# Performance work log

Measured on AMD Instinct MI355X. Metric: run time of the kernel, lower is better.

## Reference

```python
import jax, jax.numpy as jnp
import numpy as np

B, IC2, N, K = 8, 128, 2048, 32   # x: [B, 2*in_channels, N, k]
C, G = 64, 8                       # out_channels, groups
CPG = C // G                       # channels per group
EPS_BN = 1e-5


def conv1x1(x, w, b=None):
    # 1x1 conv over [B, Cin, N, K] with weight [Cout, Cin]
    y = jnp.einsum('oc,bcnk->bonk', w, x)
    if b is not None:
        y = y + b[None, :, None, None]
    return y


def bn(x, g, beta, m, v):
    # inference-mode BatchNorm2d
    scale = g / jnp.sqrt(v + EPS_BN)
    return x * scale[None, :, None, None] + (beta - m * scale)[None, :, None, None]


def lrelu(x):
    return jax.nn.leaky_relu(x, 0.2)


def setup_inputs() -> dict:
    key = jax.random.key(0)
    ks = jax.random.split(key, 32)
    d = {}
    d['x'] = jax.random.normal(ks[0], (B, IC2, N, K), jnp.float32)
    d['rel_pos'] = jax.random.normal(ks[1], (B, 3, N, K), jnp.float32)
    # pos_net
    d['pos_w1'] = jax.random.normal(ks[2], (C, 3), jnp.float32) * 0.1
    d['pos_bn_g'] = jax.random.uniform(ks[3], (C,), jnp.float32, 0.5, 1.5)
    d['pos_bn_b'] = jax.random.normal(ks[4], (C,), jnp.float32) * 0.1
    d['pos_bn_m'] = jax.random.normal(ks[5], (C,), jnp.float32) * 0.1
    d['pos_bn_v'] = jax.random.uniform(ks[6], (C,), jnp.float32, 0.5, 1.5)
    d['pos_w2'] = jax.random.normal(ks[7], (C, C), jnp.float32) * 0.1
    d['pos_b2'] = jax.random.normal(ks[8], (C,), jnp.float32) * 0.1
    # pe_proj
    d['pe_w'] = jax.random.normal(ks[9], (G, C), jnp.float32) * 0.1
    d['pe_b'] = jax.random.normal(ks[10], (G,), jnp.float32) * 0.1
    # trans (Conv+BN+LeakyReLU)
    d['trans_w'] = jax.random.normal(ks[11], (C, IC2), jnp.float32) * 0.1
    d['trans_bn_g'] = jax.random.uniform(ks[12], (C,), jnp.float32, 0.5, 1.5)
    d['trans_bn_b'] = jax.random.normal(ks[13], (C,), jnp.float32) * 0.1
    d['trans_bn_m'] = jax.random.normal(ks[14], (C,), jnp.float32) * 0.1
    d['trans_bn_v'] = jax.random.uniform(ks[15], (C,), jnp.float32, 0.5, 1.5)
    # gate_net (hidden 16)
    d['gate_w1'] = jax.random.normal(ks[16], (16, IC2), jnp.float32) * 0.1
    d['gate_bn_g'] = jax.random.uniform(ks[17], (16,), jnp.float32, 0.5, 1.5)
    d['gate_bn_b'] = jax.random.normal(ks[18], (16,), jnp.float32) * 0.1
    d['gate_bn_m'] = jax.random.normal(ks[19], (16,), jnp.float32) * 0.1
    d['gate_bn_v'] = jax.random.uniform(ks[20], (16,), jnp.float32, 0.5, 1.5)
    d['gate_w2'] = jax.random.normal(ks[21], (1, 16), jnp.float32) * 0.1
    d['gate_b2'] = jnp.full((1,), 2.0, jnp.float32)  # init.constant_(bias, 2.0)
    # attn_net (hidden C//4 = 16)
    d['attn_w1'] = jax.random.normal(ks[22], (C // 4, IC2), jnp.float32) * 0.1
    d['attn_bn_g'] = jax.random.uniform(ks[23], (C // 4,), jnp.float32, 0.5, 1.5)
    d['attn_bn_b'] = jax.random.normal(ks[24], (C // 4,), jnp.float32) * 0.1
    d['attn_bn_m'] = jax.random.normal(ks[25], (C // 4,), jnp.float32) * 0.1
    d['attn_bn_v'] = jax.random.uniform(ks[26], (C // 4,), jnp.float32, 0.5, 1.5)
    d['attn_w2'] = jax.random.normal(ks[27], (G, C // 4), jnp.float32) * 0.1
    d['attn_b2'] = jax.random.normal(ks[28], (G,), jnp.float32) * 0.1
    return d


def reference(x, rel_pos, pos_w1, pos_bn_g, pos_bn_b, pos_bn_m, pos_bn_v, pos_w2, pos_b2,
              pe_w, pe_b, trans_w, trans_bn_g, trans_bn_b, trans_bn_m, trans_bn_v,
              gate_w1, gate_bn_g, gate_bn_b, gate_bn_m, gate_bn_v, gate_w2, gate_b2,
              attn_w1, attn_bn_g, attn_bn_b, attn_bn_m, attn_bn_v, attn_w2, attn_b2):
    # pos_net: conv -> BN -> LeakyReLU -> conv(bias)
    pos_enc = conv1x1(lrelu(bn(conv1x1(rel_pos, pos_w1), pos_bn_g, pos_bn_b, pos_bn_m, pos_bn_v)),
                      pos_w2, pos_b2)                                    # [B,C,N,K]
    # trans: conv -> BN -> LeakyReLU, plus positional encoding
    trans_feat = lrelu(bn(conv1x1(x, trans_w), trans_bn_g, trans_bn_b, trans_bn_m, trans_bn_v)) + pos_enc
    # gate_net (dropout=identity in eval): -> sigmoid gate [B,1,N,K]
    gate_h = lrelu(bn(conv1x1(x, gate_w1), gate_bn_g, gate_bn_b, gate_bn_m, gate_bn_v))
    gate_map = jax.nn.sigmoid(conv1x1(gate_h, gate_w2, gate_b2))
    # attn_net -> grouped logits [B,G,N,K]
    attn_h = lrelu(bn(conv1x1(x, attn_w1), attn_bn_g, attn_bn_b, attn_bn_m, attn_bn_v))
    attn_logits = conv1x1(attn_h, attn_w2, attn_b2)
    attn_logits = attn_logits + conv1x1(pos_enc, pe_w, pe_b)             # pe_proj
    attn_logits = attn_logits + jnp.log(gate_map + 1e-6)                 # full mode: log-combine gate
    attn_w = jax.nn.softmax(attn_logits, axis=-1)                        # softmax over neighbors k
    attn_w_exp = jnp.repeat(attn_w, CPG, axis=1)                         # repeat_interleave -> [B,C,N,K]
    out_attn = jnp.sum(trans_feat * attn_w_exp, axis=-1)                 # [B,C,N]
    out_max = jnp.max(trans_feat * gate_map, axis=-1)                    # [B,C,N]
    return out_attn + out_max
```

## Files before the change

### kernel.cpp

```cpp
#include <hip/hip_runtime.h>


typedef __attribute__((ext_vector_type(8))) short bf16x8;
typedef __attribute__((ext_vector_type(4))) float f32x4;

#define EPS_BN 1e-5f

__device__ __forceinline__ unsigned pk2(float a, float b){
  unsigned ua = __float_as_uint(a) + 0x8000u;
  unsigned ub = __float_as_uint(b) + 0x8000u;
  return __builtin_amdgcn_perm(ub, ua, 0x07060302);
}
__device__ __forceinline__ short f2bf(float a){
  unsigned u = __float_as_uint(a);
  u += 0x7FFFu + ((u >> 16) & 1u);
  return (short)(u >> 16);
}
__device__ __forceinline__ float lrelu(float v){ return fmaxf(v, 0.2f*v); }

__device__ __forceinline__ void st8(short* dst, float4 a, float4 b){
  *(uint2*)(dst)     = make_uint2(pk2(a.x,a.y), pk2(a.z,a.w));
  *(uint2*)(dst + 4) = make_uint2(pk2(b.x,b.y), pk2(b.z,b.w));
}
__device__ __forceinline__ bf16x8 ld8(const short* p){
  union { bf16x8 v; uint2 q[2]; } w;
  w.q[0] = *(const uint2*)(p);
  w.q[1] = *(const uint2*)(p + 4);
  return w.v;
}

template<int N>
__device__ __forceinline__ float ror16(float x){
  return __int_as_float(__builtin_amdgcn_mov_dpp(__float_as_int(x), 0x120+N, 0xF, 0xF, false));
}
__device__ __forceinline__ float rsum16(float v){
  v += ror16<1>(v); v += ror16<2>(v); v += ror16<4>(v); v += ror16<8>(v); return v;
}
__device__ __forceinline__ float rmax16(float v){
  v = fmaxf(v, ror16<1>(v)); v = fmaxf(v, ror16<2>(v));
  v = fmaxf(v, ror16<4>(v)); v = fmaxf(v, ror16<8>(v)); return v;
}

#define MFMA16(a,b,c) __builtin_amdgcn_mfma_f32_16x16x32_bf16((a),(b),(c),0,0,0)

__global__ void gsl_prep(const float* __restrict__ pos_w2, const float* __restrict__ pe_w,
                         const float* __restrict__ pe_b,   const float* __restrict__ pos_b2,
                         float* __restrict__ ws){
  int t = threadIdx.x;
  int r = t >> 6, j = t & 63;
  float s = 0.f;
  for (int c = 0; c < 64; ++c) s += pe_w[r*64 + c] * pos_w2[c*64 + j];
  ws[t] = s;
  if (t < 16){
    float v = 0.f;
    if (t < 8){
      v = pe_b[t];
      for (int c = 0; c < 64; ++c) v += pe_w[t*64 + c] * pos_b2[c];
    }
    ws[512 + t] = v;
  }
}

__global__ __launch_bounds__(256, 2)
void gsl_fused(const float* __restrict__ x,       const float* __restrict__ rel_pos,
               const float* __restrict__ pos_w1,  const float* __restrict__ pos_g,
               const float* __restrict__ pos_bb,  const float* __restrict__ pos_m,
               const float* __restrict__ pos_v,   const float* __restrict__ pos_w2,
               const float* __restrict__ pos_b2,  const float* __restrict__ trans_w,
               const float* __restrict__ tr_g,    const float* __restrict__ tr_bb,
               const float* __restrict__ tr_m,    const float* __restrict__ tr_v,
               const float* __restrict__ gate_w1, const float* __restrict__ ga_g,
               const float* __restrict__ ga_bb,   const float* __restrict__ ga_m,
               const float* __restrict__ ga_v,    const float* __restrict__ gate_w2,
               const float* __restrict__ gate_b2, const float* __restrict__ attn_w1,
               const float* __restrict__ at_g,    const float* __restrict__ at_bb,
               const float* __restrict__ at_m,    const float* __restrict__ at_v,
               const float* __restrict__ attn_w2, const float* __restrict__ attn_b2,
               const float* __restrict__ ws,      float* __restrict__ out)
{
  __shared__ __align__(16) char smem[70784];
  short* xbuf  = (short*)smem;
  short* wmain = (short*)(smem + 33792);
  short* wpos2 = (short*)(smem + 59136);
  float* trQ  = (float*)(smem + 68928);
  float* p1T  = (float*)(smem + 69952);
  float* gaT  = (float*)(smem + 70464);
  float* atT  = (float*)(smem + 70592);

  const int tid = threadIdx.x;
  const int wv  = tid >> 6;
  const int l   = tid & 63;
  const int l15 = l & 15, g4 = l >> 4;
  const int bid = blockIdx.x;
  const int b    = bid >> 6;
  const int nblk = (bid & 63) << 5;

  if (tid < 192){
    int r = tid >> 1, c0 = (tid & 1) * 64;
    const float* src = (r < 64) ? (trans_w + r*128)
                     : (r < 80) ? (gate_w1 + (r-64)*128)
                                : (attn_w1 + (r-80)*128);
    src += c0;
    short* dst = wmain + r*132 + c0;
    #pragma unroll
    for (int j = 0; j < 8; ++j)
      st8(dst + 8*j, *(const float4*)(src + 8*j), *(const float4*)(src + 8*j + 4));
  } else {
    int r = tid - 192;
    const float* src = pos_w2 + r*64;
    short* dst = wpos2 + r*68;
    #pragma unroll
    for (int j = 0; j < 8; ++j)
      st8(dst + 8*j, *(const float4*)(src + 8*j), *(const float4*)(src + 8*j + 4));
  }
  if (tid < 16){
    int r = tid >> 1, c0 = (tid & 1) * 32;
    const float* src = ws + r*64 + c0;
    short* dst = wpos2 + (64 + r)*68 + c0;
    #pragma unroll
    for (int j = 0; j < 4; ++j)
      st8(dst + 8*j, *(const float4*)(src + 8*j), *(const float4*)(src + 8*j + 4));
  }
  if (tid < 64){
    float s = tr_g[tid] * rsqrtf(tr_v[tid] + EPS_BN);
    *(float4*)(trQ + 4*tid) = make_float4(s, tr_bb[tid] - tr_m[tid]*s, pos_b2[tid], 0.f);
    float s2 = pos_g[tid] * rsqrtf(pos_v[tid] + EPS_BN);
    p1T[2*tid] = s2; p1T[2*tid+1] = pos_bb[tid] - pos_m[tid]*s2;
  } else if (tid < 80){
    int c = tid - 64;
    float s = ga_g[c] * rsqrtf(ga_v[c] + EPS_BN);
    gaT[2*c] = s; gaT[2*c+1] = ga_bb[c] - ga_m[c]*s;
  } else if (tid < 96){
    int c = tid - 80;
    float s = at_g[c] * rsqrtf(at_v[c] + EPS_BN);
    atT[2*c] = s; atT[2*c+1] = at_bb[c] - at_m[c]*s;
  }

  uint2 pw1p[4];
  #pragma unroll
  for (int m2 = 0; m2 < 4; ++m2){
    uint2 t = make_uint2(0u, 0u);
    if (g4 == 0){
      const float* rp = pos_w1 + (16*m2 + l15)*3;
      t.x = pk2(rp[0], rp[1]);
      t.y = pk2(rp[2], 0.f);
    }
    pw1p[m2] = t;
  }
  bf16x8 gaf;
  {
    bf16x8 t = {0,0,0,0,0,0,0,0};
    #pragma unroll
    for (int j = 0; j < 8; ++j){
      int k = 8*g4 + j;
      float v2 = 0.f;
      if (l15 < 8)       { if (k >= 16) v2 = attn_w2[l15*16 + (k-16)]; }
      else if (l15 == 8) { if (k < 16)  v2 = gate_w2[k]; }
      t[j] = f2bf(v2);
    }
    gaf = t;
  }
  const float gb2v = gate_b2[0];
  float lcr[4];
  #pragma unroll
  for (int r = 0; r < 4; ++r){
    int row = 4*g4 + r;
    lcr[r] = ws[512 + row] + ((row < 8) ? attn_b2[row] : 0.f);
  }

  const int col0 = 32*wv + l15, col1 = col0 + 16;
  const int lc0 = l15, lc1 = l15 + 16;
  const int lq = l & 7, ld = l >> 3;
  const int colb = 32*wv + 4*lq;
  char*  slice = smem + wv*8448;
  short* h1b   = (short*)slice;
  short* gab   = (short*)(slice + 4352);
  const float* xp0 = x + (((long)(b*128 + 8*ld)) << 16) + colb;
  const float* rpb = rel_pos + (((long)(3*b)) << 16);
  const int och = 16*(l15 >> 2) + 4*g4 + (l15 & 3);
  float* outb = out + (((long)(b*64 + och)) << 11) + nblk + wv;

  f32x4 fa[8], fb[8];
  float rc[6] = {0.f,0.f,0.f,0.f,0.f,0.f};
  {
    const long sb0 = (long)nblk * 32;
    #pragma unroll
    for (int j = 0; j < 8; ++j) fa[j] = *(const f32x4*)(xp0 + sb0 + (((long)j) << 16));
    #pragma unroll
    for (int j = 0; j < 8; ++j) fb[j] = *(const f32x4*)(xp0 + sb0 + (((long)(64+j)) << 16));
    if (g4 == 0){
      long sg = sb0 + col0;
      rc[0] = rpb[sg];          rc[1] = rpb[sg + 65536];      rc[2] = rpb[sg + 131072];
      rc[3] = rpb[sg + 16];     rc[4] = rpb[sg + 65536 + 16]; rc[5] = rpb[sg + 131072 + 16];
    }
  }

  __syncthreads();

  for (int it = 0; it < 8; ++it){
    const long sbase = (long)nblk*32 + 128*it;

    #pragma unroll
    for (int i2 = 0; i2 < 4; ++i2){
      short* dst = xbuf + (colb+i2)*132 + 8*ld;
      *(uint2*)(dst)      = make_uint2(pk2(fa[0][i2],fa[1][i2]), pk2(fa[2][i2],fa[3][i2]));
      *(uint2*)(dst + 4)  = make_uint2(pk2(fa[4][i2],fa[5][i2]), pk2(fa[6][i2],fa[7][i2]));
      *(uint2*)(dst + 64) = make_uint2(pk2(fb[0][i2],fb[1][i2]), pk2(fb[2][i2],fb[3][i2]));
      *(uint2*)(dst + 68) = make_uint2(pk2(fb[4][i2],fb[5][i2]), pk2(fb[6][i2],fb[7][i2]));
    }

    const long nsb = sbase + 128;
    if (it < 7){
      #pragma unroll
      for (int j = 0; j < 8; ++j) fa[j] = *(const f32x4*)(xp0 + nsb + (((long)j) << 16));
    }

    f32x4 acc[6][2];
    #pragma unroll
    for (int m = 0; m < 6; ++m){
      f32x4 z = {0.f,0.f,0.f,0.f};
      acc[m][0] = z; acc[m][1] = z;
    }
    #pragma unroll
    for (int ks = 0; ks < 4; ++ks){
      bf16x8 b0 = ld8(xbuf + col0*132 + 32*ks + 8*g4);
      bf16x8 b1 = ld8(xbuf + col1*132 + 32*ks + 8*g4);
      #pragma unroll
      for (int m = 0; m < 6; ++m){
        bf16x8 af = ld8(wmain + (16*m + l15)*132 + 32*ks + 8*g4);
        acc[m][0] = MFMA16(af, b0, acc[m][0]);
        acc[m][1] = MFMA16(af, b1, acc[m][1]);
      }
    }

    if (it < 7){
      #pragma unroll
      for (int j = 0; j < 8; ++j) fb[j] = *(const f32x4*)(xp0 + nsb + (((long)(64+j)) << 16));
    }

    {
      bf16x8 rf0 = {0,0,0,0,0,0,0,0}, rf1 = {0,0,0,0,0,0,0,0};
      if (g4 == 0){
        union { bf16x8 v; unsigned u[4]; } t0, t1;
        t0.u[0] = pk2(rc[0], rc[1]); t0.u[1] = pk2(rc[2], 0.f); t0.u[2] = 0u; t0.u[3] = 0u;
        t1.u[0] = pk2(rc[3], rc[4]); t1.u[1] = pk2(rc[5], 0.f); t1.u[2] = 0u; t1.u[3] = 0u;
        rf0 = t0.v; rf1 = t1.v;
      }
      #pragma unroll
      for (int m2 = 0; m2 < 4; ++m2){
        union { bf16x8 v; unsigned u[4]; } aw;
        aw.u[0] = pw1p[m2].x; aw.u[1] = pw1p[m2].y; aw.u[2] = 0u; aw.u[3] = 0u;
        f32x4 z = {0.f,0.f,0.f,0.f};
        f32x4 d0 = MFMA16(aw.v, rf0, z);
        f32x4 d1 = MFMA16(aw.v, rf1, z);
        int cb2 = 16*m2 + 4*g4;
        float2 t0 = *(const float2*)(p1T + 2*(cb2+0));
        float2 t1 = *(const float2*)(p1T + 2*(cb2+1));
        float2 t2 = *(const float2*)(p1T + 2*(cb2+2));
        float2 t3 = *(const float2*)(p1T + 2*(cb2+3));
        float h0 = lrelu(t0.x*d0[0]+t0.y), h1v = lrelu(t1.x*d0[1]+t1.y);
        float h2 = lrelu(t2.x*d0[2]+t2.y), h3 = lrelu(t3.x*d0[3]+t3.y);
        *(uint2*)(h1b + lc0*68 + cb2) = make_uint2(pk2(h0,h1v), pk2(h2,h3));
        h0 = lrelu(t0.x*d1[0]+t0.y); h1v = lrelu(t1.x*d1[1]+t1.y);
        h2 = lrelu(t2.x*d1[2]+t2.y); h3 = lrelu(t3.x*d1[3]+t3.y);
        *(uint2*)(h1b + lc1*68 + cb2) = make_uint2(pk2(h0,h1v), pk2(h2,h3));
      }
    }
    if (g4 == 0 && it < 7){
      long sg = nsb + col0;
      rc[0] = rpb[sg];          rc[1] = rpb[sg + 65536];      rc[2] = rpb[sg + 131072];
      rc[3] = rpb[sg + 16];     rc[4] = rpb[sg + 65536 + 16]; rc[5] = rpb[sg + 131072 + 16];
    }

    #pragma unroll
    for (int m = 0; m < 4; ++m)
      #pragma unroll
      for (int r = 0; r < 4; ++r){
        float4 tq = *(const float4*)(trQ + 4*(16*m + 4*g4 + r));
        acc[m][0][r] = lrelu(tq.x*acc[m][0][r] + tq.y) + tq.z;
        acc[m][1][r] = lrelu(tq.x*acc[m][1][r] + tq.y) + tq.z;
      }

    f32x4 pac4[2];
    {
      f32x4 z = {0.f,0.f,0.f,0.f};
      pac4[0] = z; pac4[1] = z;
    }
    #pragma unroll
    for (int ks = 0; ks < 2; ++ks){
      bf16x8 h0 = ld8(h1b + lc0*68 + 32*ks + 8*g4);
      bf16x8 h1v = ld8(h1b + lc1*68 + 32*ks + 8*g4);
      #pragma unroll
      for (int m2 = 0; m2 < 4; ++m2){
        bf16x8 af = ld8(wpos2 + (16*m2 + l15)*68 + 32*ks + 8*g4);
        acc[m2][0] = MFMA16(af, h0, acc[m2][0]);
        acc[m2][1] = MFMA16(af, h1v, acc[m2][1]);
      }
      bf16x8 af4 = ld8(wpos2 + (64 + l15)*68 + 32*ks + 8*g4);
      pac4[0] = MFMA16(af4, h0, pac4[0]);
      pac4[1] = MFMA16(af4, h1v, pac4[1]);
    }

    {
      int hc = 4*g4;
      float2 g0p = *(const float2*)(gaT + 2*(hc+0));
      float2 g1p = *(const float2*)(gaT + 2*(hc+1));
      float2 g2p = *(const float2*)(gaT + 2*(hc+2));
      float2 g3p = *(const float2*)(gaT + 2*(hc+3));
      float2 a0p = *(const float2*)(atT + 2*(hc+0));
      float2 a1p = *(const float2*)(atT + 2*(hc+1));
      float2 a2p = *(const float2*)(atT + 2*(hc+2));
      float2 a3p = *(const float2*)(atT + 2*(hc+3));
      #pragma unroll
      for (int ct = 0; ct < 2; ++ct){
        int lc = (ct == 0) ? lc0 : lc1;
        float q0 = lrelu(g0p.x*acc[4][ct][0] + g0p.y), q1 = lrelu(g1p.x*acc[4][ct][1] + g1p.y);
        float q2 = lrelu(g2p.x*acc[4][ct][2] + g2p.y), q3 = lrelu(g3p.x*acc[4][ct][3] + g3p.y);
        *(uint2*)(gab + lc*36 + hc) = make_uint2(pk2(q0,q1), pk2(q2,q3));
        float a0 = lrelu(a0p.x*acc[5][ct][0] + a0p.y), a1 = lrelu(a1p.x*acc[5][ct][1] + a1p.y);
        float a2 = lrelu(a2p.x*acc[5][ct][2] + a2p.y), a3 = lrelu(a3p.x*acc[5][ct][3] + a3p.y);
        *(uint2*)(gab + lc*36 + 16 + hc) = make_uint2(pk2(a0,a1), pk2(a2,a3));
      }
    }

    f32x4 gac0 = {0.f,0.f,0.f,0.f}, gac1 = gac0;
    {
      bf16x8 g0 = ld8(gab + lc0*36 + 8*g4);
      bf16x8 g1 = ld8(gab + lc1*36 + 8*g4);
      gac0 = MFMA16(gaf, g0, gac0);
      gac1 = MFMA16(gaf, g1, gac1);
    }

    float gv0 = __shfl(gac0[0], 32 + l15, 64);
    float gv1 = __shfl(gac1[0], 32 + l15, 64);
    float gm0 = 1.f/(1.f + __expf(-(gv0 + gb2v)));
    float gm1 = 1.f/(1.f + __expf(-(gv1 + gb2v)));
    float lg0 = __logf(gm0 + 1e-6f), lg1 = __logf(gm1 + 1e-6f);

    float wg0[4], wg1[4];
    #pragma unroll
    for (int r = 0; r < 4; ++r){
      float t0 = gac0[r] + pac4[0][r] + lcr[r] + lg0;
      float t1 = gac1[r] + pac4[1][r] + lcr[r] + lg1;
      float mx = rmax16(fmaxf(t0, t1));
      float e0 = __expf(t0 - mx), e1 = __expf(t1 - mx);
      float inv = 1.f / rsum16(e0 + e1);
      wg0[r] = e0 * inv; wg1[r] = e1 * inv;
    }

    float vA[16], vM[16];
    const bool hi = (g4 >= 2);
    #pragma unroll
    for (int m = 0; m < 4; ++m){
      int src = 16*(m >> 1) + l15;
      float a0 = __shfl(wg0[(2*m) & 3],   src, 64);
      float b0 = __shfl(wg0[(2*m+1) & 3], src, 64);
      float a1 = __shfl(wg1[(2*m) & 3],   src, 64);
      float b1 = __shfl(wg1[(2*m+1) & 3], src, 64);
      float w0 = hi ? b0 : a0;
      float w1 = hi ? b1 : a1;
      #pragma unroll
      for (int r = 0; r < 4; ++r){
        vA[4*m+r] = acc[m][0][r]*w0 + acc[m][1][r]*w1;
        vM[4*m+r] = fmaxf(acc[m][0][r]*gm0, acc[m][1][r]*gm1);
      }
    }
    #pragma unroll
    for (int s = 0; s < 4; ++s){
      const int mm = 8 >> s;
      const bool up = (l15 & mm) != 0;
      #pragma unroll
      for (int k2 = 0; k2 < mm; ++k2){
        float sendA = up ? vA[k2] : vA[k2 + mm];
        float keepA = up ? vA[k2 + mm] : vA[k2];
        vA[k2] = keepA + __shfl_xor(sendA, mm, 64);
        float sendM = up ? vM[k2] : vM[k2 + mm];
        float keepM = up ? vM[k2 + mm] : vM[k2];
        vM[k2] = fmaxf(keepM, __shfl_xor(sendM, mm, 64));
      }
    }
    outb[4*it] = vA[0] + vM[0];
  }
}

extern "C" void kernel_launch(void* const* d_in, const int* in_sizes, int n_in,
                              void* d_out, int out_size, void* d_ws, size_t ws_size,
                              hipStream_t stream){
  (void)in_sizes; (void)n_in; (void)out_size; (void)ws_size;
  gsl_prep<<<dim3(1), dim3(512), 0, stream>>>(
    (const float*)d_in[7], (const float*)d_in[9], (const float*)d_in[10],
    (const float*)d_in[8], (float*)d_ws);
  gsl_fused<<<dim3(512), dim3(256), 0, stream>>>(
    (const float*)d_in[0],  (const float*)d_in[1],  (const float*)d_in[2],
    (const float*)d_in[3],  (const float*)d_in[4],  (const float*)d_in[5],
    (const float*)d_in[6],  (const float*)d_in[7],  (const float*)d_in[8],
    (const float*)d_in[11], (const float*)d_in[12], (const float*)d_in[13],
    (const float*)d_in[14], (const float*)d_in[15], (const float*)d_in[16],
    (const float*)d_in[17], (const float*)d_in[18], (const float*)d_in[19],
    (const float*)d_in[20], (const float*)d_in[21], (const float*)d_in[22],
    (const float*)d_in[23], (const float*)d_in[24], (const float*)d_in[25],
    (const float*)d_in[26], (const float*)d_in[27], (const float*)d_in[28],
    (const float*)d_in[29], (const float*)d_ws, (float*)d_out);
}
```

Measured before the change: 70.02 us.

## Pre-swizzle bf16 weight fragments in prep kernel, halve LDS, double grid

The prep kernel now converts all conv weights (trans/gate/attn, pos_w2, fused pe projection, pos_w1, gate/attn second layer) to bf16 in MFMA fragment order in the workspace. The fused kernel reads these fragments directly from global/L2 instead of staging them in LDS. That cuts LDS from about 70KB to 35KB so three blocks can fit per CU. The grid doubles to 1024 blocks with 4 iterations each, and the next-tile prefetch moves later in the loop. The cost is per-iteration global/L2 weight loads inside the MFMA loop instead of LDS reads, plus a heavier single-block prep kernel.

```diff
diff --git a/kernel.cpp b/kernel.cpp
--- a/kernel.cpp
+++ b/kernel.cpp
@@ -5,23 +5,21 @@
 typedef __attribute__((ext_vector_type(4))) float f32x4;
 
 #define EPS_BN 1e-5f
+
+#define WSA   0
+#define WSP   24576
+#define WSPE  32768
+#define WSPW1 34816
+#define WSGAF 36864
+#define WSLCR 37888
 
 __device__ __forceinline__ unsigned pk2(float a, float b){
   unsigned ua = __float_as_uint(a) + 0x8000u;
   unsigned ub = __float_as_uint(b) + 0x8000u;
   return __builtin_amdgcn_perm(ub, ua, 0x07060302);
 }
-__device__ __forceinline__ short f2bf(float a){
-  unsigned u = __float_as_uint(a);
-  u += 0x7FFFu + ((u >> 16) & 1u);
-  return (short)(u >> 16);
-}
 __device__ __forceinline__ float lrelu(float v){ return fmaxf(v, 0.2f*v); }
 
-__device__ __forceinline__ void st8(short* dst, float4 a, float4 b){
-  *(uint2*)(dst)     = make_uint2(pk2(a.x,a.y), pk2(a.z,a.w));
-  *(uint2*)(dst + 4) = make_uint2(pk2(b.x,b.y), pk2(b.z,b.w));
-}
 __device__ __forceinline__ bf16x8 ld8(const short* p){
   union { bf16x8 v; uint2 q[2]; } w;
   w.q[0] = *(const uint2*)(p);
@@ -43,84 +41,113 @@
 
 #define MFMA16(a,b,c) __builtin_amdgcn_mfma_f32_16x16x32_bf16((a),(b),(c),0,0,0)
 
-__global__ void gsl_prep(const float* __restrict__ pos_w2, const float* __restrict__ pe_w,
-                         const float* __restrict__ pe_b,   const float* __restrict__ pos_b2,
-                         float* __restrict__ ws){
-  int t = threadIdx.x;
-  int r = t >> 6, j = t & 63;
-  float s = 0.f;
-  for (int c = 0; c < 64; ++c) s += pe_w[r*64 + c] * pos_w2[c*64 + j];
-  ws[t] = s;
+__global__ void gsl_prep(const float* __restrict__ trans_w, const float* __restrict__ gate_w1,
+                         const float* __restrict__ attn_w1, const float* __restrict__ pos_w2,
+                         const float* __restrict__ pe_w,    const float* __restrict__ pe_b,
+                         const float* __restrict__ pos_b2,  const float* __restrict__ pos_w1,
+                         const float* __restrict__ gate_w2, const float* __restrict__ attn_w2,
+                         const float* __restrict__ attn_b2, char* __restrict__ ws){
+  const int t = threadIdx.x;
+  for (int idx = t; idx < 1536; idx += 512){
+    int id = idx >> 6, lane = idx & 63;
+    int m = id >> 2, ks = id & 3, l15 = lane & 15, g4 = lane >> 4;
+    const float* src = (m < 4)  ? (trans_w + (16*m + l15)*128)
+                     : (m == 4) ? (gate_w1 + l15*128)
+                                : (attn_w1 + l15*128);
+    src += 32*ks + 8*g4;
+    uint4 u;
+    u.x = pk2(src[0],src[1]); u.y = pk2(src[2],src[3]);
+    u.z = pk2(src[4],src[5]); u.w = pk2(src[6],src[7]);
+    *(uint4*)(ws + WSA + idx*16) = u;
+  }
+  {
+    int id = t >> 6, lane = t & 63, l15 = lane & 15, g4 = lane >> 4;
+    const float* src = pos_w2 + (16*(id>>1) + l15)*64 + 32*(id&1) + 8*g4;
+    uint4 u;
+    u.x = pk2(src[0],src[1]); u.y = pk2(src[2],src[3]);
+    u.z = pk2(src[4],src[5]); u.w = pk2(src[6],src[7]);
+    *(uint4*)(ws + WSP + t*16) = u;
+  }
+  if (t < 128){
+    int ks = t >> 6, lane = t & 63, l15 = lane & 15, g4 = lane >> 4;
+    uint4 u = make_uint4(0u,0u,0u,0u);
+    if (l15 < 8){
+      float w[8];
+      #pragma unroll
+      for (int j = 0; j < 8; ++j){
+        int c = 32*ks + 8*g4 + j;
+        float s = 0.f;
+        for (int k = 0; k < 64; ++k) s += pe_w[l15*64 + k] * pos_w2[k*64 + c];
+        w[j] = s;
+      }
+      u.x = pk2(w[0],w[1]); u.y = pk2(w[2],w[3]);
+      u.z = pk2(w[4],w[5]); u.w = pk2(w[6],w[7]);
+    }
+    *(uint4*)(ws + WSPE + t*16) = u;
+  }
+  if (t < 256){
+    int m2 = t >> 6, lane = t & 63, l15 = lane & 15, g4 = lane >> 4;
+    uint2 u = make_uint2(0u, 0u);
+    if (g4 == 0){
+      const float* rp = pos_w1 + (16*m2 + l15)*3;
+      u.x = pk2(rp[0], rp[1]); u.y = pk2(rp[2], 0.f);
+    }
+    *(uint2*)(ws + WSPW1 + t*8) = u;
+  }
+  if (t < 64){
+    int l15 = t & 15, g4 = t >> 4;
+    float v[8];
+    #pragma unroll
+    for (int j = 0; j < 8; ++j){
+      int k = 8*g4 + j;
+      float v2 = 0.f;
+      if (l15 < 8)       { if (k >= 16) v2 = attn_w2[l15*16 + (k-16)]; }
+      else if (l15 == 8) { if (k < 16)  v2 = gate_w2[k]; }
+      v[j] = v2;
+    }
+    uint4 u;
+    u.x = pk2(v[0],v[1]); u.y = pk2(v[2],v[3]);
+    u.z = pk2(v[4],v[5]); u.w = pk2(v[6],v[7]);
+    *(uint4*)(ws + WSGAF + t*16) = u;
+  }
   if (t < 16){
     float v = 0.f;
     if (t < 8){
-      v = pe_b[t];
+      v = pe_b[t] + attn_b2[t];
       for (int c = 0; c < 64; ++c) v += pe_w[t*64 + c] * pos_b2[c];
     }
-    ws[512 + t] = v;
-  }
-}
-
-__global__ __launch_bounds__(256, 2)
-void gsl_fused(const float* __restrict__ x,       const float* __restrict__ rel_pos,
-               const float* __restrict__ pos_w1,  const float* __restrict__ pos_g,
-               const float* __restrict__ pos_bb,  const float* __restrict__ pos_m,
-               const float* __restrict__ pos_v,   const float* __restrict__ pos_w2,
-               const float* __restrict__ pos_b2,  const float* __restrict__ trans_w,
-               const float* __restrict__ tr_g,    const float* __restrict__ tr_bb,
-               const float* __restrict__ tr_m,    const float* __restrict__ tr_v,
-               const float* __restrict__ gate_w1, const float* __restrict__ ga_g,
-               const float* __restrict__ ga_bb,   const float* __restrict__ ga_m,
-               const float* __restrict__ ga_v,    const float* __restrict__ gate_w2,
-               const float* __restrict__ gate_b2, const float* __restrict__ attn_w1,
-               const float* __restrict__ at_g,    const float* __restrict__ at_bb,
-               const float* __restrict__ at_m,    const float* __restrict__ at_v,
-               const float* __restrict__ attn_w2, const float* __restrict__ attn_b2,
-               const float* __restrict__ ws,      float* __restrict__ out)
+    *(float*)(ws + WSLCR + t*4) = v;
+  }
+}
+
+__global__ __launch_bounds__(256, 3)
+void gsl_fused(const float* __restrict__ x,      const float* __restrict__ rel_pos,
+               const float* __restrict__ pos_g,  const float* __restrict__ pos_bb,
+               const float* __restrict__ pos_m,  const float* __restrict__ pos_v,
+               const float* __restrict__ pos_b2, const float* __restrict__ tr_g,
+               const float* __restrict__ tr_bb,  const float* __restrict__ tr_m,
+               const float* __restrict__ tr_v,   const float* __restrict__ ga_g,
+               const float* __restrict__ ga_bb,  const float* __restrict__ ga_m,
+               const float* __restrict__ ga_v,   const float* __restrict__ gate_b2,
+               const float* __restrict__ at_g,   const float* __restrict__ at_bb,
+               const float* __restrict__ at_m,   const float* __restrict__ at_v,
+               const char* __restrict__ ws,      float* __restrict__ out)
 {
-  __shared__ __align__(16) char smem[70784];
-  short* xbuf  = (short*)smem;
-  short* wmain = (short*)(smem + 33792);
-  short* wpos2 = (short*)(smem + 59136);
-  float* trQ  = (float*)(smem + 68928);
-  float* p1T  = (float*)(smem + 69952);
-  float* gaT  = (float*)(smem + 70464);
-  float* atT  = (float*)(smem + 70592);
+  __shared__ __align__(16) char smem[35584];
+  short* xbuf = (short*)smem;
+  float* trQ  = (float*)(smem + 33792);
+  float* p1T  = (float*)(smem + 34816);
+  float* gaT  = (float*)(smem + 35328);
+  float* atT  = (float*)(smem + 35456);
 
   const int tid = threadIdx.x;
   const int wv  = tid >> 6;
   const int l   = tid & 63;
   const int l15 = l & 15, g4 = l >> 4;
   const int bid = blockIdx.x;
-  const int b    = bid >> 6;
-  const int nblk = (bid & 63) << 5;
-
-  if (tid < 192){
-    int r = tid >> 1, c0 = (tid & 1) * 64;
-    const float* src = (r < 64) ? (trans_w + r*128)
-                     : (r < 80) ? (gate_w1 + (r-64)*128)
-                                : (attn_w1 + (r-80)*128);
-    src += c0;
-    short* dst = wmain + r*132 + c0;
-    #pragma unroll
-    for (int j = 0; j < 8; ++j)
-      st8(dst + 8*j, *(const float4*)(src + 8*j), *(const float4*)(src + 8*j + 4));
-  } else {
-    int r = tid - 192;
-    const float* src = pos_w2 + r*64;
-    short* dst = wpos2 + r*68;
-    #pragma unroll
-    for (int j = 0; j < 8; ++j)
-      st8(dst + 8*j, *(const float4*)(src + 8*j), *(const float4*)(src + 8*j + 4));
-  }
-  if (tid < 16){
-    int r = tid >> 1, c0 = (tid & 1) * 32;
-    const float* src = ws + r*64 + c0;
-    short* dst = wpos2 + (64 + r)*68 + c0;
-    #pragma unroll
-    for (int j = 0; j < 4; ++j)
-      st8(dst + 8*j, *(const float4*)(src + 8*j), *(const float4*)(src + 8*j + 4));
-  }
+  const int b    = bid >> 7;
+  const int nblk = (bid & 127) << 4;
+
   if (tid < 64){
     float s = tr_g[tid] * rsqrtf(tr_v[tid] + EPS_BN);
     *(float4*)(trQ + 4*tid) = make_float4(s, tr_bb[tid] - tr_m[tid]*s, pos_b2[tid], 0.f);
@@ -138,35 +165,14 @@
 
   uint2 pw1p[4];
   #pragma unroll
-  for (int m2 = 0; m2 < 4; ++m2){
-    uint2 t = make_uint2(0u, 0u);
-    if (g4 == 0){
-      const float* rp = pos_w1 + (16*m2 + l15)*3;
-      t.x = pk2(rp[0], rp[1]);
-      t.y = pk2(rp[2], 0.f);
-    }
-    pw1p[m2] = t;
-  }
-  bf16x8 gaf;
-  {
-    bf16x8 t = {0,0,0,0,0,0,0,0};
-    #pragma unroll
-    for (int j = 0; j < 8; ++j){
-      int k = 8*g4 + j;
-      float v2 = 0.f;
-      if (l15 < 8)       { if (k >= 16) v2 = attn_w2[l15*16 + (k-16)]; }
-      else if (l15 == 8) { if (k < 16)  v2 = gate_w2[k]; }
-      t[j] = f2bf(v2);
-    }
-    gaf = t;
-  }
-  const float gb2v = gate_b2[0];
+  for (int m2 = 0; m2 < 4; ++m2)
+    pw1p[m2] = *(const uint2*)(ws + WSPW1 + (m2*64 + l)*8);
+  bf16x8 gaf = *(const bf16x8*)(ws + WSGAF + l*16);
   float lcr[4];
   #pragma unroll
-  for (int r = 0; r < 4; ++r){
-    int row = 4*g4 + r;
-    lcr[r] = ws[512 + row] + ((row < 8) ? attn_b2[row] : 0.f);
-  }
+  for (int r = 0; r < 4; ++r)
+    lcr[r] = *(const float*)(ws + WSLCR + (4*g4 + r)*4);
+  const float gb2v = gate_b2[0];
 
   const int col0 = 32*wv + l15, col1 = col0 + 16;
   const int lc0 = l15, lc1 = l15 + 16;
@@ -197,7 +203,7 @@
 
   __syncthreads();
 
-  for (int it = 0; it < 8; ++it){
+  for (int it = 0; it < 4; ++it){
     const long sbase = (long)nblk*32 + 128*it;
 
     #pragma unroll
@@ -209,12 +215,6 @@
       *(uint2*)(dst + 68) = make_uint2(pk2(fb[4][i2],fb[5][i2]), pk2(fb[6][i2],fb[7][i2]));
     }
 
-    const long nsb = sbase + 128;
-    if (it < 7){
-      #pragma unroll
-      for (int j = 0; j < 8; ++j) fa[j] = *(const f32x4*)(xp0 + nsb + (((long)j) << 16));
-    }
-
     f32x4 acc[6][2];
     #pragma unroll
     for (int m = 0; m < 6; ++m){
@@ -227,15 +227,10 @@
       bf16x8 b1 = ld8(xbuf + col1*132 + 32*ks + 8*g4);
       #pragma unroll
       for (int m = 0; m < 6; ++m){
-        bf16x8 af = ld8(wmain + (16*m + l15)*132 + 32*ks + 8*g4);
+        bf16x8 af = *(const bf16x8*)(ws + WSA + (((m<<2)|ks)*64 + l)*16);
         acc[m][0] = MFMA16(af, b0, acc[m][0]);
         acc[m][1] = MFMA16(af, b1, acc[m][1]);
       }
-    }
-
-    if (it < 7){
-      #pragma unroll
-      for (int j = 0; j < 8; ++j) fb[j] = *(const f32x4*)(xp0 + nsb + (((long)(64+j)) << 16));
     }
 
     {
@@ -266,11 +261,6 @@
         *(uint2*)(h1b + lc1*68 + cb2) = make_uint2(pk2(h0,h1v), pk2(h2,h3));
       }
     }
-    if (g4 == 0 && it < 7){
-      long sg = nsb + col0;
-      rc[0] = rpb[sg];          rc[1] = rpb[sg + 65536];      rc[2] = rpb[sg + 131072];
-      rc[3] = rpb[sg + 16];     rc[4] = rpb[sg + 65536 + 16]; rc[5] = rpb[sg + 131072 + 16];
-    }
 
     #pragma unroll
     for (int m = 0; m < 4; ++m)
@@ -292,13 +282,26 @@
       bf16x8 h1v = ld8(h1b + lc1*68 + 32*ks + 8*g4);
       #pragma unroll
       for (int m2 = 0; m2 < 4; ++m2){
-        bf16x8 af = ld8(wpos2 + (16*m2 + l15)*68 + 32*ks + 8*g4);
+        bf16x8 af = *(const bf16x8*)(ws + WSP + ((m2*2 + ks)*64 + l)*16);
         acc[m2][0] = MFMA16(af, h0, acc[m2][0]);
         acc[m2][1] = MFMA16(af, h1v, acc[m2][1]);
       }
-      bf16x8 af4 = ld8(wpos2 + (64 + l15)*68 + 32*ks + 8*g4);
+      bf16x8 af4 = *(const bf16x8*)(ws + WSPE + (ks*64 + l)*16);
       pac4[0] = MFMA16(af4, h0, pac4[0]);
       pac4[1] = MFMA16(af4, h1v, pac4[1]);
+    }
+
+    if (it < 3){
+      const long nsb = sbase + 128;
+      #pragma unroll
+      for (int j = 0; j < 8; ++j) fa[j] = *(const f32x4*)(xp0 + nsb + (((long)j) << 16));
+      #pragma unroll
+      for (int j = 0; j < 8; ++j) fb[j] = *(const f32x4*)(xp0 + nsb + (((long)(64+j)) << 16));
+      if (g4 == 0){
+        long sg = nsb + col0;
+        rc[0] = rpb[sg];          rc[1] = rpb[sg + 65536];      rc[2] = rpb[sg + 131072];
+        rc[3] = rpb[sg + 16];     rc[4] = rpb[sg + 65536 + 16]; rc[5] = rpb[sg + 131072 + 16];
+      }
     }
 
     {
@@ -388,17 +391,17 @@
                               hipStream_t stream){
   (void)in_sizes; (void)n_in; (void)out_size; (void)ws_size;
   gsl_prep<<<dim3(1), dim3(512), 0, stream>>>(
-    (const float*)d_in[7], (const float*)d_in[9], (const float*)d_in[10],
-    (const float*)d_in[8], (float*)d_ws);
-  gsl_fused<<<dim3(512), dim3(256), 0, stream>>>(
-    (const float*)d_in[0],  (const float*)d_in[1],  (const float*)d_in[2],
-    (const float*)d_in[3],  (const float*)d_in[4],  (const float*)d_in[5],
-    (const float*)d_in[6],  (const float*)d_in[7],  (const float*)d_in[8],
-    (const float*)d_in[11], (const float*)d_in[12], (const float*)d_in[13],
-    (const float*)d_in[14], (const float*)d_in[15], (const float*)d_in[16],
-    (const float*)d_in[17], (const float*)d_in[18], (const float*)d_in[19],
-    (const float*)d_in[20], (const float*)d_in[21], (const float*)d_in[22],
-    (const float*)d_in[23], (const float*)d_in[24], (const float*)d_in[25],
-    (const float*)d_in[26], (const float*)d_in[27], (const float*)d_in[28],
-    (const float*)d_in[29], (const float*)d_ws, (float*)d_out);
-}
+    (const float*)d_in[11], (const float*)d_in[16], (const float*)d_in[23],
+    (const float*)d_in[7],  (const float*)d_in[9],  (const float*)d_in[10],
+    (const float*)d_in[8],  (const float*)d_in[2],  (const float*)d_in[21],
+    (const float*)d_in[28], (const float*)d_in[29], (char*)d_ws);
+  gsl_fused<<<dim3(1024), dim3(256), 0, stream>>>(
+    (const float*)d_in[0],  (const float*)d_in[1],  (const float*)d_in[3],
+    (const float*)d_in[4],  (const float*)d_in[5],  (const float*)d_in[6],
+    (const float*)d_in[8],  (const float*)d_in[12], (const float*)d_in[13],
+    (const float*)d_in[14], (const float*)d_in[15], (const float*)d_in[17],
+    (const float*)d_in[18], (const float*)d_in[19], (const float*)d_in[20],
+    (const float*)d_in[22], (const float*)d_in[24], (const float*)d_in[25],
+    (const float*)d_in[26], (const float*)d_in[27], (const char*)d_ws,
+    (float*)d_out);
+}
```

Measured after the change: 263.6 us. 276% more time.
